# Optimization experiments

Measured on AMD Instinct MI355X. Metric: run time of the kernel, lower is better.

The kernel has to match this reference:

```python
import jax, jax.numpy as jnp
import numpy as np

N_NODES = 5
B, C, H, W = 4, 256, 32, 32
THRESH = 0.3
EPS = 1e-12


def setup_inputs() -> dict:
    key = jax.random.key(0)
    k1, k2, k3, k4 = jax.random.split(key, 4)
    x = jax.random.normal(k1, (N_NODES, B, C, H, W), dtype=jnp.float32)
    w = jax.random.normal(k2, (N_NODES, N_NODES), dtype=jnp.float32)
    # 5 stacked conv1x1 'experts': Conv2d(2C -> C, k=1) weight [C,2C] + bias [C]
    conv_w = jax.random.normal(k3, (N_NODES, C, 2 * C), dtype=jnp.float32) * 0.02
    conv_b = jax.random.normal(k4, (N_NODES, C), dtype=jnp.float32) * 0.02
    return {"x": x, "w": w, "conv_w": conv_w, "conv_b": conv_b}


def reference(x, w, conv_w, conv_b):
    # x: [N, B, C, H, W] -- the list of N node feature maps stacked
    N, b, c, h, ww = x.shape
    P = b * c * h * ww  # 'pixels' = total element count of one node tensor

    # conv_i(cat(node_j, node_i + node_j)) splits into W1@node_j + W2@(node_i+node_j) + b_i
    W1 = conv_w[:, :, :c]          # [N, C, C] acts on node_j
    W2 = conv_w[:, :, c:]          # [N, C, C] acts on node_i + node_j
    A = W1 + W2                    # combined weight on node_j

    term_j = jnp.einsum('ick,jbkhw->ijbchw', A, x)    # [N,N,B,C,H,W]
    term_i = jnp.einsum('ick,ibkhw->ibchw', W2, x)    # [N,B,C,H,W]
    target = term_j + term_i[:, None] + conv_b[:, None, None, :, None, None]
    distance = x[None, :] - target                    # distance[i,j] = node_j - conv_i(...)

    # edge_list[:, i, j] = flatten(distance[i, j])  -> [P, N, N]
    edge = distance.reshape(N, N, P).transpose(2, 0, 1)

    # new_edge = edge * w; sigmoid; threshold at 0.3; L2-normalize over dim=2 (j axis)
    e = jax.nn.sigmoid(edge * w)
    e = jnp.where(e > THRESH, e, jnp.zeros_like(e))
    norm = jnp.sqrt(jnp.sum(e * e, axis=2, keepdims=True))
    e = e / jnp.maximum(norm, EPS)

    # node matrix: [P, N] of flattened node features; fuse h[p,i] = sum_j e[p,i,j]*node[p,j]
    node = x.reshape(N, P).T
    hmat = jnp.einsum('pij,pj->pi', e, node)          # [P, N]
    return hmat.T.reshape(N, b, c, h, ww)
```

## Files before the change

kernel.cpp:

```cpp
#include <hip/hip_runtime.h>
#include <cmath>

#define NN  5
#define BB  4
#define CCH 256
#define HWD 1024
#define THRESH_V 0.3f
#define EPS_V 1e-12f


#define CT 64
#define WT 64
#define KC 16
#define APAD 68
#define SPAD 68

#define W2T_OFF (NN * CCH * CCH)

#define XS_FLOATS (NN * KC * WT)
#define AS_OFF    XS_FLOATS
#define W2S_OFF   (AS_OFF + KC * APAD)
#define SMEM_FLOATS (W2S_OFF + KC * APAD)

__global__ void fub_prep(const float* __restrict__ conv_w, float* __restrict__ ws)
{
    const int t = blockIdx.x * 256 + threadIdx.x;
    if (t >= NN * CCH * 64) return;
    const int c4 = (t & 63) << 2;
    const int k  = (t >> 6) & 255;
    const int i  = t >> 14;
    float s1[4], s2[4];
#pragma unroll
    for (int cc = 0; cc < 4; ++cc) {
        const float* p = conv_w + (size_t)(i * CCH + c4 + cc) * (2 * CCH) + k;
        const float w1 = p[0];
        const float w2 = p[CCH];
        s1[cc] = w1 + w2;
        s2[cc] = w2;
    }
    float* At  = ws + (size_t)(i * CCH + k) * CCH + c4;
    float* W2t = ws + W2T_OFF + (size_t)(i * CCH + k) * CCH + c4;
    *(float4*)At  = make_float4(s1[0], s1[1], s1[2], s1[3]);
    *(float4*)W2t = make_float4(s2[0], s2[1], s2[2], s2[3]);
}

__global__ __launch_bounds__(384, 3)
void fub_main(const float* __restrict__ x, const float* __restrict__ wmat,
              const float* __restrict__ ws, const float* __restrict__ conv_b,
              float* __restrict__ out)
{
    __shared__ __align__(16) float smem[SMEM_FLOATS];
    float* Xs  = smem;
    float* As  = smem + AS_OFF;
    float* W2s = smem + W2S_OFF;
    float* Es  = smem;

    const int tid  = threadIdx.x;
    const int wv   = tid >> 6;
    const int lane = tid & 63;

    const int wg  = blockIdx.x;
    int L = (wg & 7) * 160 + (wg >> 3);
    const int i   = L % 5;  L /= 5;
    const int ct  = L & 3;  L >>= 2;
    const int b   = L & 3;  L >>= 2;
    const int hwt = L;

    const int c0  = ct * CT;
    const int hw0 = hwt * WT;

    const int lr = (lane >> 3) << 3;
    const int lc = (lane & 7)  << 3;

    const int jx = (wv < NN) ? wv : i;
    const float* Ms = (wv == 5) ? W2s : As;
    const float* Mb = Ms + lr;
    const float* Xb = Xs + jx * (KC * WT) + lc;

    float acc[8][8];
#pragma unroll
    for (int r = 0; r < 8; ++r)
#pragma unroll
        for (int c = 0; c < 8; ++c) acc[r][c] = 0.0f;

    for (int k0 = 0; k0 < CCH; k0 += KC) {
        if (tid < 256) {
#pragma unroll
            for (int it = 0; it < 5; ++it) {
                const int t   = tid + it * 256;
                const int j   = t >> 8;
                const int rem = t & 255;
                const int kk  = rem >> 4;
                const int q4  = (rem & 15) << 2;
                const float4 v = *(const float4*)(
                    x + (size_t)((j * BB + b) * CCH + k0 + kk) * HWD + hw0 + q4);
                *(float4*)(Xs + j * (KC * WT) + kk * WT + q4) = v;
            }
        } else {
            const int u = tid - 256;
#pragma unroll
            for (int it = 0; it < 4; ++it) {
                const int t   = u + it * 128;
                const int tbl = t >> 8;
                const int rem = t & 255;
                const int kk  = rem >> 4;
                const int c4  = (rem & 15) << 2;
                const float4 v = *(const float4*)(
                    ws + (size_t)(tbl ? W2T_OFF : 0)
                       + (size_t)(i * CCH + k0 + kk) * CCH + c0 + c4);
                *(float4*)((tbl ? W2s : As) + kk * APAD + c4) = v;
            }
        }
        __syncthreads();

#pragma unroll 4
        for (int kk = 0; kk < KC; ++kk) {
            const float4 a0 = *(const float4*)(Mb + kk * APAD);
            const float4 a1 = *(const float4*)(Mb + kk * APAD + 4);
            const float4 x0 = *(const float4*)(Xb + kk * WT);
            const float4 x1 = *(const float4*)(Xb + kk * WT + 4);
            const float ar[8] = {a0.x, a0.y, a0.z, a0.w, a1.x, a1.y, a1.z, a1.w};
            const float xc[8] = {x0.x, x0.y, x0.z, x0.w, x1.x, x1.y, x1.z, x1.w};
#pragma unroll
            for (int r = 0; r < 8; ++r)
#pragma unroll
                for (int c = 0; c < 8; ++c)
                    acc[r][c] = fmaf(ar[r], xc[c], acc[r][c]);
        }
        __syncthreads();
    }

    const int rhme  = lr >> 4;
    const int rbase = lr & 15;

    float wrow[NN];
#pragma unroll
    for (int j = 0; j < NN; ++j) wrow[j] = wmat[i * NN + j];

#pragma unroll
    for (int rh = 0; rh < 4; ++rh) {
        if (rhme == rh) {
            float* Eb = Es + wv * (16 * SPAD) + lc;
#pragma unroll
            for (int r = 0; r < 8; ++r) {
                *(float4*)(Eb + (rbase + r) * SPAD) =
                    make_float4(acc[r][0], acc[r][1], acc[r][2], acc[r][3]);
                *(float4*)(Eb + (rbase + r) * SPAD + 4) =
                    make_float4(acc[r][4], acc[r][5], acc[r][6], acc[r][7]);
            }
        }
        __syncthreads();

        if (tid < 256) {
            const int row  = tid >> 4;
            const int colq = (tid & 15) << 2;
            const int c    = c0 + rh * 16 + row;
            const float bias = conv_b[i * CCH + c];

            const float4 T = *(const float4*)(Es + 5 * (16 * SPAD) + row * SPAD + colq);
            const float Tv[4] = {T.x, T.y, T.z, T.w};

            float num[4] = {0.f, 0.f, 0.f, 0.f};
            float sq [4] = {0.f, 0.f, 0.f, 0.f};
#pragma unroll
            for (int j = 0; j < NN; ++j) {
                const float4 s  = *(const float4*)(Es + j * (16 * SPAD) + row * SPAD + colq);
                const float4 xj = *(const float4*)(
                    x + (size_t)((j * BB + b) * CCH + c) * HWD + hw0 + colq);
                const float sv[4] = {s.x, s.y, s.z, s.w};
                const float xv[4] = {xj.x, xj.y, xj.z, xj.w};
#pragma unroll
                for (int cc = 0; cc < 4; ++cc) {
                    const float target = sv[cc] + Tv[cc] + bias;
                    const float dist   = xv[cc] - target;
                    const float z      = dist * wrow[j];
                    float e = 1.0f / (1.0f + expf(-z));
                    e = (e > THRESH_V) ? e : 0.0f;
                    sq[cc]  = fmaf(e, e, sq[cc]);
                    num[cc] = fmaf(e, xv[cc], num[cc]);
                }
            }
            float4 res;
            res.x = num[0] / fmaxf(sqrtf(sq[0]), EPS_V);
            res.y = num[1] / fmaxf(sqrtf(sq[1]), EPS_V);
            res.z = num[2] / fmaxf(sqrtf(sq[2]), EPS_V);
            res.w = num[3] / fmaxf(sqrtf(sq[3]), EPS_V);
            *(float4*)(out + (size_t)((i * BB + b) * CCH + c) * HWD + hw0 + colq) = res;
        }
        __syncthreads();
    }
}

extern "C" void kernel_launch(void* const* d_in, const int* in_sizes, int n_in,
                              void* d_out, int out_size, void* d_ws, size_t ws_size,
                              hipStream_t stream) {
    const float* x      = (const float*)d_in[0];
    const float* w      = (const float*)d_in[1];
    const float* conv_w = (const float*)d_in[2];
    const float* conv_b = (const float*)d_in[3];
    float* out = (float*)d_out;
    float* ws  = (float*)d_ws;

    fub_prep<<<dim3(320), dim3(256), 0, stream>>>(conv_w, ws);

    fub_main<<<dim3(1280), dim3(384), 0, stream>>>(x, w, ws, conv_b, out);
}
```

Baseline: 328.1 us.

## Emulate fp32 GEMM with split-bf16 MFMA plus exact recompute near threshold

Replaces the scalar FMA GEMM with bf16 MFMA instructions, splitting each fp32 weight and activation into three bf16 parts and summing six cross products to recover near-fp32 accuracy. New prep kernels pre-split and pre-swizzle the weights and x into MFMA fragment layout in workspace. Where the sigmoid output lands within a small guard band of the threshold, the value is recomputed exactly in fp32, so the hard threshold decision stays correct. This adds two extra prep passes, extra workspace traffic, and a divergent slow path. The new path is taken only if the workspace is large enough, otherwise the old kernel runs.

```diff
diff --git a/kernel.cpp b/kernel.cpp
--- a/kernel.cpp
+++ b/kernel.cpp
@@ -7,16 +7,264 @@
 #define HWD 1024
 #define THRESH_V 0.3f
 #define EPS_V 1e-12f
-
+#define GUARD 3e-4f
+
+
+typedef __attribute__((ext_vector_type(8))) short          bf16x8;
+typedef __attribute__((ext_vector_type(8))) unsigned short u16x8;
+typedef __attribute__((ext_vector_type(4))) float          f32x4;
+
+#define AUNITS      (NN * 2 * 3 * 16 * 8 * 64)
+#define XBASE       AUNITS
+#define XUNITS      (NN * BB * 3 * 64 * 8 * 64)
+#define WS_MFMA_BYTES ((size_t)(AUNITS + XUNITS) * 16)
+
+#define SPAD 68
+#define ES_FLOATS (6 * 32 * SPAD)
+
+__device__ __forceinline__ unsigned short f2bf(float f) {
+    unsigned int u = __float_as_uint(f);
+    unsigned int r = (u + 0x7fffu + ((u >> 16) & 1u)) >> 16;
+    return (unsigned short)r;
+}
+__device__ __forceinline__ float bf2f(unsigned short h) {
+    return __uint_as_float(((unsigned int)h) << 16);
+}
+__device__ __forceinline__ void split3(float v, unsigned short& h,
+                                       unsigned short& m, unsigned short& l) {
+    h = f2bf(v);
+    const float r1 = v - bf2f(h);
+    m = f2bf(r1);
+    const float r2 = r1 - bf2f(m);
+    l = f2bf(r2);
+}
+
+__device__ __attribute__((noinline))
+float exact_e(const float* __restrict__ x, const float* __restrict__ conv_w,
+              int i, int jn, int b, int c, int hw, float bias, float wij)
+{
+    const float* cw = conv_w + (size_t)(i * CCH + c) * (2 * CCH);
+    const float* xj = x + (size_t)((jn * BB + b) * CCH) * HWD + hw;
+    const float* xi = x + (size_t)((i  * BB + b) * CCH) * HWD + hw;
+    float S = 0.f, T = 0.f;
+    for (int k = 0; k < CCH; ++k) {
+        const float A = cw[k] + cw[CCH + k];
+        S = fmaf(A,            xj[(size_t)k * HWD], S);
+        T = fmaf(cw[CCH + k],  xi[(size_t)k * HWD], T);
+    }
+    const float xv     = xj[(size_t)c * HWD];
+    const float target = S + T + bias;
+    const float dist   = xv - target;
+    const float z      = dist * wij;
+    return 1.0f / (1.0f + expf(-z));
+}
+
+__global__ void fub_prep_a6(const float* __restrict__ conv_w, u16x8* __restrict__ W)
+{
+    const int t = blockIdx.x * 256 + threadIdx.x;
+    if (t >= NN * 16 * 8 * 64) return;
+    const int lane  = t & 63;
+    const int kst   = (t >> 6) & 7;
+    const int mg    = (t >> 9) & 15;
+    const int i     = t >> 13;
+
+    const int c  = mg * 16 + (lane & 15);
+    const int kb = kst * 32 + 8 * (lane >> 4);
+
+    u16x8 A[3], Wv[3];
+#pragma unroll
+    for (int jj = 0; jj < 8; ++jj) {
+        const float* p = conv_w + (size_t)(i * CCH + c) * (2 * CCH) + kb + jj;
+        const float w1 = p[0];
+        const float w2 = p[CCH];
+        unsigned short h, m, l;
+        split3(w1 + w2, h, m, l);
+        A[0][jj] = h; A[1][jj] = m; A[2][jj] = l;
+        split3(w2, h, m, l);
+        Wv[0][jj] = h; Wv[1][jj] = m; Wv[2][jj] = l;
+    }
+#pragma unroll
+    for (int hl = 0; hl < 3; ++hl) {
+        const int fA = (((i * 2 + 0) * 3 + hl) * 16 + mg) * 8 + kst;
+        const int fW = (((i * 2 + 1) * 3 + hl) * 16 + mg) * 8 + kst;
+        W[fA * 64 + lane] = A[hl];
+        W[fW * 64 + lane] = Wv[hl];
+    }
+}
+
+__global__ void fub_prep_x6(const float* __restrict__ x, u16x8* __restrict__ W)
+{
+    const int t = blockIdx.x * 256 + threadIdx.x;
+    const int lane = t & 63;
+    const int kst  = (t >> 6) & 7;
+    const int pg   = (t >> 9) & 63;
+    const int b    = (t >> 15) & 3;
+    const int j    = t >> 17;
+    if (j >= NN) return;
+
+    const int p  = pg * 16 + (lane & 15);
+    const int kb = kst * 32 + 8 * (lane >> 4);
+
+    u16x8 X[3];
+#pragma unroll
+    for (int jj = 0; jj < 8; ++jj) {
+        const float v = x[(size_t)((j * BB + b) * CCH + kb + jj) * HWD + p];
+        unsigned short h, m, l;
+        split3(v, h, m, l);
+        X[0][jj] = h; X[1][jj] = m; X[2][jj] = l;
+    }
+#pragma unroll
+    for (int hl = 0; hl < 3; ++hl) {
+        const int f = (((j * BB + b) * 3 + hl) * 64 + pg) * 8 + kst;
+        W[XBASE + f * 64 + lane] = X[hl];
+    }
+}
+
+__global__ __launch_bounds__(384, 2)
+void fub_main_mfma(const float* __restrict__ x, const float* __restrict__ wmat,
+                   const bf16x8* __restrict__ AT, const float* __restrict__ conv_b,
+                   const float* __restrict__ conv_w, float* __restrict__ out)
+{
+    __shared__ __align__(16) float Es[ES_FLOATS];
+
+    const int tid  = threadIdx.x;
+    const int wv   = tid >> 6;
+    const int lane = tid & 63;
+
+    const int wg  = blockIdx.x;
+    int L = (wg & 7) * 160 + (wg >> 3);
+    const int i   = L % 5;  L /= 5;
+    const int ct  = L & 3;  L >>= 2;
+    const int b   = L & 3;  L >>= 2;
+    const int hwt = L;
+
+    const int c0  = ct * 64;
+    const int hw0 = hwt * 64;
+    const int mg0 = ct * 4;
+    const int pg0 = hwt * 4;
+
+    const int m  = (wv == 5) ? 1 : 0;
+    const int jx = (wv < NN) ? wv : i;
+
+    const int baseA = ((((i * 2 + m) * 3 + 0) * 16 + mg0) * 8) * 64 + lane;
+    const int baseX = XBASE + ((((jx * BB + b) * 3 + 0) * 64 + pg0) * 8) * 64 + lane;
+
+    f32x4 acc[4][4];
+#pragma unroll
+    for (int mf = 0; mf < 4; ++mf)
+#pragma unroll
+        for (int nf = 0; nf < 4; ++nf) acc[mf][nf] = (f32x4){0.f, 0.f, 0.f, 0.f};
+
+#pragma unroll 1
+    for (int kst = 0; kst < 8; ++kst) {
+        bf16x8 xh[4], xm[4], xl[4];
+#pragma unroll
+        for (int f = 0; f < 4; ++f) {
+            const int o = (f * 8 + kst) * 64;
+            xh[f] = AT[baseX + o];
+            xm[f] = AT[baseX + 32768 + o];
+            xl[f] = AT[baseX + 65536 + o];
+        }
+#pragma unroll
+        for (int mf = 0; mf < 4; ++mf) {
+            const int o = (mf * 8 + kst) * 64;
+            const bf16x8 ah = AT[baseA + o];
+            const bf16x8 am = AT[baseA + 8192 + o];
+            const bf16x8 al = AT[baseA + 16384 + o];
+#pragma unroll
+            for (int nf = 0; nf < 4; ++nf) {
+                f32x4 a = acc[mf][nf];
+                a = __builtin_amdgcn_mfma_f32_16x16x32_bf16(ah, xh[nf], a, 0, 0, 0);
+                a = __builtin_amdgcn_mfma_f32_16x16x32_bf16(am, xh[nf], a, 0, 0, 0);
+                a = __builtin_amdgcn_mfma_f32_16x16x32_bf16(ah, xm[nf], a, 0, 0, 0);
+                a = __builtin_amdgcn_mfma_f32_16x16x32_bf16(am, xm[nf], a, 0, 0, 0);
+                a = __builtin_amdgcn_mfma_f32_16x16x32_bf16(ah, xl[nf], a, 0, 0, 0);
+                a = __builtin_amdgcn_mfma_f32_16x16x32_bf16(al, xh[nf], a, 0, 0, 0);
+                acc[mf][nf] = a;
+            }
+        }
+    }
+
+    float wrow[NN];
+#pragma unroll
+    for (int j = 0; j < NN; ++j) wrow[j] = wmat[i * NN + j];
+
+    const int g16 = lane >> 4;
+    const int n16 = lane & 15;
+
+#pragma unroll
+    for (int rh = 0; rh < 2; ++rh) {
+#pragma unroll
+        for (int mh = 0; mh < 2; ++mh) {
+            const int mf = 2 * rh + mh;
+            float* Eb = Es + wv * (32 * SPAD) + (mh * 16 + 4 * g16) * SPAD + n16;
+#pragma unroll
+            for (int nf = 0; nf < 4; ++nf) {
+                const f32x4 v = acc[mf][nf];
+                float* E = Eb + nf * 16;
+                E[0 * SPAD] = v.x;
+                E[1 * SPAD] = v.y;
+                E[2 * SPAD] = v.z;
+                E[3 * SPAD] = v.w;
+            }
+        }
+        __syncthreads();
+
+        if (tid < 256) {
+            const int row  = tid >> 3;
+            const int col8 = (tid & 7) << 3;
+            const int c    = c0 + rh * 32 + row;
+            const float bias = conv_b[i * CCH + c];
+
+#pragma unroll
+            for (int h = 0; h < 2; ++h) {
+                const int colq = col8 + 4 * h;
+
+                const float4 T = *(const float4*)(Es + 5 * (32 * SPAD) + row * SPAD + colq);
+                const float Tv[4] = {T.x, T.y, T.z, T.w};
+
+                float num[4] = {0.f, 0.f, 0.f, 0.f};
+                float sq [4] = {0.f, 0.f, 0.f, 0.f};
+#pragma unroll
+                for (int j = 0; j < NN; ++j) {
+                    const float4 s  = *(const float4*)(Es + j * (32 * SPAD) + row * SPAD + colq);
+                    const float4 xj = *(const float4*)(
+                        x + (size_t)((j * BB + b) * CCH + c) * HWD + hw0 + colq);
+                    const float sv[4] = {s.x, s.y, s.z, s.w};
+                    const float xv[4] = {xj.x, xj.y, xj.z, xj.w};
+#pragma unroll
+                    for (int cc = 0; cc < 4; ++cc) {
+                        const float target = sv[cc] + Tv[cc] + bias;
+                        const float dist   = xv[cc] - target;
+                        const float z      = dist * wrow[j];
+                        float e = 1.0f / (1.0f + expf(-z));
+                        if (__builtin_expect(fabsf(e - THRESH_V) < GUARD, 0)) {
+                            e = exact_e(x, conv_w, i, j, b, c,
+                                        hw0 + colq + cc, bias, wrow[j]);
+                        }
+                        e = (e > THRESH_V) ? e : 0.0f;
+                        sq[cc]  = fmaf(e, e, sq[cc]);
+                        num[cc] = fmaf(e, xv[cc], num[cc]);
+                    }
+                }
+                float4 res;
+                res.x = num[0] / fmaxf(sqrtf(sq[0]), EPS_V);
+                res.y = num[1] / fmaxf(sqrtf(sq[1]), EPS_V);
+                res.z = num[2] / fmaxf(sqrtf(sq[2]), EPS_V);
+                res.w = num[3] / fmaxf(sqrtf(sq[3]), EPS_V);
+                *(float4*)(out + (size_t)((i * BB + b) * CCH + c) * HWD + hw0 + colq) =
+                    res;
+            }
+        }
+        __syncthreads();
+    }
+}
 
 #define CT 64
 #define WT 64
 #define KC 16
 #define APAD 68
-#define SPAD 68
-
 #define W2T_OFF (NN * CCH * CCH)
-
 #define XS_FLOATS (NN * KC * WT)
 #define AS_OFF    XS_FLOATS
 #define W2S_OFF   (AS_OFF + KC * APAD)
@@ -45,9 +293,9 @@
 }
 
 __global__ __launch_bounds__(384, 3)
-void fub_main(const float* __restrict__ x, const float* __restrict__ wmat,
-              const float* __restrict__ ws, const float* __restrict__ conv_b,
-              float* __restrict__ out)
+void fub_main_r8(const float* __restrict__ x, const float* __restrict__ wmat,
+                 const float* __restrict__ ws, const float* __restrict__ conv_b,
+                 float* __restrict__ out)
 {
     __shared__ __align__(16) float smem[SMEM_FLOATS];
     float* Xs  = smem;
@@ -199,9 +447,16 @@
     const float* conv_w = (const float*)d_in[2];
     const float* conv_b = (const float*)d_in[3];
     float* out = (float*)d_out;
-    float* ws  = (float*)d_ws;
-
-    fub_prep<<<dim3(320), dim3(256), 0, stream>>>(conv_w, ws);
-
-    fub_main<<<dim3(1280), dim3(384), 0, stream>>>(x, w, ws, conv_b, out);
-}
+
+    if (ws_size >= WS_MFMA_BYTES) {
+        u16x8* W = (u16x8*)d_ws;
+        fub_prep_a6<<<dim3(160),  dim3(256), 0, stream>>>(conv_w, W);
+        fub_prep_x6<<<dim3(2560), dim3(256), 0, stream>>>(x, W);
+        fub_main_mfma<<<dim3(1280), dim3(384), 0, stream>>>(
+            x, w, (const bf16x8*)d_ws, conv_b, conv_w, out);
+    } else {
+        float* ws = (float*)d_ws;
+        fub_prep<<<dim3(320), dim3(256), 0, stream>>>(conv_w, ws);
+        fub_main_r8<<<dim3(1280), dim3(384), 0, stream>>>(x, w, ws, conv_b, out);
+    }
+}
```

Measured after the change: 710.8 us. +116.6%, slower.
